# Kernel tuning notes

Hardware: AMD Instinct MI355X
Metric: run time of the kernel (lower is better)

The kernel has to match this reference:

```python
import jax, jax.numpy as jnp
import numpy as np

DIM, K, B, H, W = 256, 7, 16, 56, 56
EPS = 1e-5

def _conv(x, w, pad, groups=1):
    return jax.lax.conv_general_dilated(
        x, w, window_strides=(1, 1), padding=[(pad, pad), (pad, pad)],
        dimension_numbers=('NCHW', 'OIHW', 'NCHW'), feature_group_count=groups)

def _bn(x, g, b, m, v):
    scale = g / jnp.sqrt(v + EPS)          # [C]
    bias = b - m * scale
    return x * scale[None, :, None, None] + bias[None, :, None, None]

def _silu(x):
    return x * jax.nn.sigmoid(x)

def setup_inputs() -> dict:
    key = jax.random.key(0)
    ks = jax.random.split(key, 12)
    f = lambda k_, shp, s=0.05: jax.random.normal(k_, shp, jnp.float32) * s
    d = {
        'x':   jax.random.normal(ks[0], (B, DIM, H, W), jnp.float32),
        # RepConv branch: dense 3x3 conv + BN, dense 1x1 conv + BN
        'w3':  f(ks[1], (DIM, DIM, 3, 3)),
        'g1':  1.0 + f(ks[2], (DIM,)), 'b1': f(ks[3], (DIM,)),
        'm1':  f(ks[4], (DIM,)),       'v1': jax.random.uniform(ks[4], (DIM,), jnp.float32) + 0.5,
        'w1':  f(ks[5], (DIM, DIM, 1, 1)),
        'g2':  1.0 + f(ks[6], (DIM,)), 'b2': f(ks[7], (DIM,)),
        'm2':  f(ks[8], (DIM,)),       'v2': jax.random.uniform(ks[8], (DIM,), jnp.float32) + 0.5,
        # depthwise branches
        'dw7': f(ks[9], (DIM, 1, 7, 7)),
        'dwk': f(ks[10], (DIM, 1, K, K)),
        # final BN
        'g3':  1.0 + f(ks[11], (DIM,)), 'b3': f(ks[11], (DIM,)),
        'm3':  f(ks[11], (DIM,)),       'v3': jax.random.uniform(ks[11], (DIM,), jnp.float32) + 0.5,
    }
    return d

def reference(x, w3, g1, b1, m1, v1, w1, g2, b2, m2, v2, dw7, dwk, g3, b3, m3, v3):
    # RepConv (train-mode, bn=False): SiLU(BN(conv3x3(x)) + BN(conv1x1(x)))
    rep = _silu(_bn(_conv(x, w3, 1), g1, b1, m1, v1)
                + _bn(_conv(x, w1, 0), g2, b2, m2, v2))
    # parallel depthwise branches
    y = rep + _conv(x, dw7, 3, groups=DIM) + _conv(x, dwk, K // 2, groups=DIM)
    return _silu(_bn(y, g3, b3, m3, v3))
```

## Files before the change

### kernel.cpp

```cpp
#include <hip/hip_runtime.h>
#include <stdint.h>
#include <stddef.h>

#define DIM 256
#define NB 16
#define HH 56
#define WW 56
#define HWP (HH*WW)
#define PH 62
#define PW 62
#define NPIX (NB*HWP)
#define EPSV 1e-5f

using f32x4  = __attribute__((ext_vector_type(4))) float;
using bf16x8 = __attribute__((ext_vector_type(8))) __bf16;

static __device__ __forceinline__ unsigned short f2bf(float f) {
    union { float f; unsigned u; } v; v.f = f;
    unsigned r = v.u + 0x7FFFu + ((v.u >> 16) & 1u);
    return (unsigned short)(r >> 16);
}
static __device__ __forceinline__ float bf2f(unsigned short u) {
    union { unsigned u; float f; } v; v.u = ((unsigned)u) << 16; return v.f;
}
static __device__ __forceinline__ float silu_f(float z) {
    return z / (1.f + __expf(-z));
}

__global__ void prep_weights(
    const float* __restrict__ w3, const float* __restrict__ g1, const float* __restrict__ b1,
    const float* __restrict__ m1, const float* __restrict__ v1, const float* __restrict__ w1,
    const float* __restrict__ g2, const float* __restrict__ b2, const float* __restrict__ m2,
    const float* __restrict__ v2, const float* __restrict__ dw7, const float* __restrict__ dwk,
    const float* __restrict__ g3, const float* __restrict__ b3, const float* __restrict__ m3,
    const float* __restrict__ v3,
    unsigned short* __restrict__ WkT, float* __restrict__ dwm, float* __restrict__ biasm,
    float* __restrict__ sc3, float* __restrict__ bi3)
{
    int co = blockIdx.x, t = threadIdx.x;
    float s1 = g1[co] * rsqrtf(v1[co] + EPSV);
    float s2 = g2[co] * rsqrtf(v2[co] + EPSV);
    float w1v = w1[co*DIM + t] * s2;
    const float* w3r = w3 + (size_t)(co*DIM + t)*9;
#pragma unroll
    for (int s = 0; s < 9; ++s) {
        float v = w3r[s]*s1 + (s == 4 ? w1v : 0.f);
        WkT[((size_t)s*DIM + co)*DIM + t] = f2bf(v);
    }
    if (t < 49) dwm[co*49 + t] = dw7[co*49 + t] + dwk[co*49 + t];
    if (t == 0) {
        biasm[co] = (b1[co] - m1[co]*s1) + (b2[co] - m2[co]*s2);
        float s3 = g3[co] * rsqrtf(v3[co] + EPSV);
        sc3[co] = s3;
        bi3[co] = b3[co] - m3[co]*s3;
    }
}

__global__ void prep_xpad(const float* __restrict__ x, unsigned short* __restrict__ xpad)
{
    __shared__ float lds[64][57];
    int cc = blockIdx.x;
    int ph = blockIdx.y;
    int b  = blockIdx.z;
    int t  = threadIdx.x;
    int c0 = cc*64;
    char* rowc = (char*)xpad + ((size_t)(b*PH + ph)*PW)*(DIM*2) + c0*2;

    if (ph < 3 || ph >= HH + 3) {
        uint4 z = {0u,0u,0u,0u};
#pragma unroll
        for (int j = 0; j < 2; ++j) {
            int idx = j*256 + t;
            if (idx < 496) {
                int pix = idx >> 3, q = idx & 7;
                *(uint4*)(rowc + (size_t)pix*(DIM*2) + q*16) = z;
            }
        }
        return;
    }
    if (t < 48) {
        int p = t >> 3, q = t & 7;
        int pw = (p < 3) ? p : (PW - 6 + p);
        uint4 z = {0u,0u,0u,0u};
        *(uint4*)(rowc + (size_t)pw*(DIM*2) + q*16) = z;
    }
    int h = ph - 3;
#pragma unroll
    for (int j = 0; j < 14; ++j) {
        int idx = j*256 + t;
        int c = idx / 56, w = idx % 56;
        lds[c][w] = x[((size_t)(b*DIM + c0 + c)*HH + h)*WW + w];
    }
    __syncthreads();
#pragma unroll
    for (int j = 0; j < 7; ++j) {
        int idx = j*256 + t;
        int w = idx >> 5, cp = idx & 31;
        unsigned lo = f2bf(lds[2*cp][w]);
        unsigned hi = f2bf(lds[2*cp+1][w]);
        unsigned val = lo | (hi << 16);
        *(unsigned*)(rowc + (size_t)(w + 3)*(DIM*2) + 4*cp) = val;
    }
}

__global__ void depthwise7(const float* __restrict__ x, const float* __restrict__ dwm,
                           unsigned short* __restrict__ dwout)
{
    __shared__ float plane[PH*PW];
    int c = blockIdx.x, b = blockIdx.y, t = threadIdx.x;
    const float* xp = x + ((size_t)b*DIM + c)*HWP;
    float wr[49];
#pragma unroll
    for (int i = 0; i < 49; ++i) wr[i] = dwm[c*49 + i];
#pragma unroll
    for (int j = 0; j < 16; ++j) {
        int idx = j*256 + t;
        if (idx < PH*PW) {
            int ph = idx / PW, pw = idx % PW;
            int h = ph - 3, w = pw - 3;
            float v = 0.f;
            if ((unsigned)h < HH && (unsigned)w < WW) v = xp[h*WW + w];
            plane[idx] = v;
        }
    }
    __syncthreads();
    unsigned short* op = dwout + ((size_t)b*DIM + c)*HWP;
#pragma unroll
    for (int j = 0; j < 4; ++j) {
        int q = j*256 + t;
        if (q < 784) {
            int h = q / 14, w0 = (q % 14)*4;
            float a0=0.f, a1=0.f, a2=0.f, a3=0.f;
#pragma unroll
            for (int dy = 0; dy < 7; ++dy) {
                float row[10];
#pragma unroll
                for (int i = 0; i < 10; ++i) row[i] = plane[(h+dy)*PW + w0 + i];
#pragma unroll
                for (int dx = 0; dx < 7; ++dx) {
                    float wv = wr[dy*7 + dx];
                    a0 += row[dx]   * wv;
                    a1 += row[dx+1] * wv;
                    a2 += row[dx+2] * wv;
                    a3 += row[dx+3] * wv;
                }
            }
            uint2 pk;
            pk.x = (unsigned)f2bf(a0) | ((unsigned)f2bf(a1) << 16);
            pk.y = (unsigned)f2bf(a2) | ((unsigned)f2bf(a3) << 16);
            *(uint2*)&op[h*WW + w0] = pk;
        }
    }
}

__global__ __launch_bounds__(256, 2)
void main_conv(const unsigned short* __restrict__ xpad, const unsigned short* __restrict__ WkT,
               const unsigned short* __restrict__ dwo, const float* __restrict__ biasm,
               const float* __restrict__ sc3, const float* __restrict__ bi3,
               float* __restrict__ out)
{
    __shared__ __align__(16) char smem[65536];
    int t = threadIdx.x;
    int lane = t & 63, wv = t >> 6;
    int wm = wv >> 1, wn = wv & 1;
    int qm = lane & 15, qg = lane >> 4;

    int swz = (((lane & 7) ^ ((lane >> 3) & 7)) << 4);

    uintptr_t gA[4], gB[4];
#pragma unroll
    for (int r = 0; r < 4; ++r) {
        int pixt = r*32 + wv*8 + (lane >> 3);
        int P = blockIdx.x*128 + pixt;
        int bb = P / HWP, rem = P % HWP;
        int h = rem / WW, w = rem % WW;
        gA[r] = (uintptr_t)xpad + ((size_t)((bb*PH + h + 2)*PW + (w + 2))*DIM)*2 + swz;
        int cog = blockIdx.y*128 + pixt;
        gB[r] = (uintptr_t)WkT + ((size_t)cog*DIM)*2 + swz;
    }

    f32x4 acc[4][4] = {};

    auto stage = [&](int s, int buf) {
        int s9 = s >> 2, ch = s & 3;
        int ky = s9 / 3, kx = s9 - ky*3;
        int offA = (ky*PW + kx)*(DIM*2) + ch*128;
        int offB = s9*(DIM*DIM*2) + ch*128;
        char* base = smem + buf*32768;
#pragma unroll
        for (int r = 0; r < 4; ++r) {
            __builtin_amdgcn_global_load_lds(
                (const __attribute__((address_space(1))) void*)(gA[r] + offA),
                (__attribute__((address_space(3))) void*)(base + (r*32 + wv*8)*128),
                16, 0, 0);
            __builtin_amdgcn_global_load_lds(
                (const __attribute__((address_space(1))) void*)(gB[r] + offB),
                (__attribute__((address_space(3))) void*)(base + 16384 + (r*32 + wv*8)*128),
                16, 0, 0);
        }
    };

    int kxo = (qg << 4) ^ ((lane & 7) << 4);
    auto compute = [&](int buf) {
        const char* pA = smem + buf*32768 + (wm*64 + qm)*128;
        const char* pB = smem + buf*32768 + 16384 + (wn*64 + qm)*128;
#pragma unroll
        for (int kk = 0; kk < 2; ++kk) {
            int ko = kxo ^ (kk << 6);
            bf16x8 a[4], b[4];
#pragma unroll
            for (int i = 0; i < 4; ++i) {
                a[i] = *(const bf16x8*)(pA + i*2048 + ko);
                b[i] = *(const bf16x8*)(pB + i*2048 + ko);
            }
#pragma unroll
            for (int i = 0; i < 4; ++i)
#pragma unroll
                for (int j = 0; j < 4; ++j)
                    acc[i][j] = __builtin_amdgcn_mfma_f32_16x16x32_bf16(a[i], b[j], acc[i][j], 0, 0, 0);
        }
    };

    stage(0, 0);
    __syncthreads();
#pragma unroll 1
    for (int it = 0; it < 18; ++it) {
        stage(2*it + 1, 1);
        compute(0);
        __syncthreads();
        if (it < 17) stage(2*it + 2, 0);
        compute(1);
        __syncthreads();
    }

    float* ep = (float*)smem + wv*1088;
#pragma unroll
    for (int mi = 0; mi < 4; ++mi) {
#pragma unroll
        for (int ni = 0; ni < 4; ++ni)
#pragma unroll
            for (int r = 0; r < 4; ++r)
                ep[(ni*16 + qm)*17 + 4*qg + r] = acc[mi][ni][r];
        __syncthreads();
        int P = blockIdx.x*128 + wm*64 + mi*16 + qm;
        int bb = P / HWP, rem = P % HWP;
        size_t obase = (size_t)bb*DIM*HWP + rem;
#pragma unroll
        for (int j = 0; j < 16; ++j) {
            int col = j*4 + qg;
            int cog = blockIdx.y*128 + wn*64 + col;
            float z = ep[col*17 + qm] + biasm[cog];
            float rep = silu_f(z);
            float y = rep + bf2f(dwo[obase + (size_t)cog*HWP]);
            float yy = y * sc3[cog] + bi3[cog];
            out[obase + (size_t)cog*HWP] = silu_f(yy);
        }
        __syncthreads();
    }
}

extern "C" void kernel_launch(void* const* d_in, const int* in_sizes, int n_in,
                              void* d_out, int out_size, void* d_ws, size_t ws_size,
                              hipStream_t stream)
{
    (void)in_sizes; (void)n_in; (void)out_size; (void)ws_size;
    const float* x   = (const float*)d_in[0];
    const float* w3  = (const float*)d_in[1];
    const float* g1  = (const float*)d_in[2];
    const float* b1  = (const float*)d_in[3];
    const float* m1  = (const float*)d_in[4];
    const float* v1  = (const float*)d_in[5];
    const float* w1  = (const float*)d_in[6];
    const float* g2  = (const float*)d_in[7];
    const float* b2  = (const float*)d_in[8];
    const float* m2  = (const float*)d_in[9];
    const float* v2  = (const float*)d_in[10];
    const float* dw7 = (const float*)d_in[11];
    const float* dwk = (const float*)d_in[12];
    const float* g3  = (const float*)d_in[13];
    const float* b3  = (const float*)d_in[14];
    const float* m3  = (const float*)d_in[15];
    const float* v3  = (const float*)d_in[16];
    float* out = (float*)d_out;

    char* ws = (char*)d_ws;
    unsigned short* xpad = (unsigned short*)(ws);
    unsigned short* WkT  = (unsigned short*)(ws + 31490048);
    unsigned short* dwo  = (unsigned short*)(ws + 32669696);
    float* dwm   = (float*)(ws + 58359808);
    float* biasm = (float*)(ws + 58409984);
    float* sc3   = (float*)(ws + 58411008);
    float* bi3   = (float*)(ws + 58412032);

    prep_weights<<<dim3(DIM), dim3(256), 0, stream>>>(
        w3, g1, b1, m1, v1, w1, g2, b2, m2, v2, dw7, dwk, g3, b3, m3, v3,
        WkT, dwm, biasm, sc3, bi3);
    prep_xpad<<<dim3(4, PH, NB), dim3(256), 0, stream>>>(x, xpad);
    depthwise7<<<dim3(DIM, NB), dim3(256), 0, stream>>>(x, dwm, dwo);
    main_conv<<<dim3(NPIX/128, 2), dim3(256), 0, stream>>>(xpad, WkT, dwo, biasm, sc3, bi3, out);
}
```

Before: 166.3 us.

## Enlarge main conv block tile to 256x256 with eight waves and finer waits

```diff
diff --git a/kernel.cpp b/kernel.cpp
--- a/kernel.cpp
+++ b/kernel.cpp
@@ -153,109 +153,122 @@
     }
 }
 
-__global__ __launch_bounds__(256, 2)
+__global__ __launch_bounds__(512, 2)
 void main_conv(const unsigned short* __restrict__ xpad, const unsigned short* __restrict__ WkT,
                const unsigned short* __restrict__ dwo, const float* __restrict__ biasm,
                const float* __restrict__ sc3, const float* __restrict__ bi3,
                float* __restrict__ out)
 {
-    __shared__ __align__(16) char smem[65536];
+    __shared__ __align__(16) char smem[131072];
     int t = threadIdx.x;
     int lane = t & 63, wv = t >> 6;
-    int wm = wv >> 1, wn = wv & 1;
+    int wm = wv >> 2, wn = wv & 3;
     int qm = lane & 15, qg = lane >> 4;
-
-    int swz = (((lane & 7) ^ ((lane >> 3) & 7)) << 4);
+    int bx = blockIdx.x;
+
+    int swz = (((t & 7) ^ ((t >> 3) & 7)) << 4);
 
     uintptr_t gA[4], gB[4];
 #pragma unroll
-    for (int r = 0; r < 4; ++r) {
-        int pixt = r*32 + wv*8 + (lane >> 3);
-        int P = blockIdx.x*128 + pixt;
+    for (int p = 0; p < 4; ++p) {
+        int row = p*64 + (t >> 3);
+        int P = bx*256 + row;
         int bb = P / HWP, rem = P % HWP;
         int h = rem / WW, w = rem % WW;
-        gA[r] = (uintptr_t)xpad + ((size_t)((bb*PH + h + 2)*PW + (w + 2))*DIM)*2 + swz;
-        int cog = blockIdx.y*128 + pixt;
-        gB[r] = (uintptr_t)WkT + ((size_t)cog*DIM)*2 + swz;
-    }
-
-    f32x4 acc[4][4] = {};
+        gA[p] = (uintptr_t)xpad + ((size_t)((bb*PH + h + 2)*PW + (w + 2))*DIM)*2 + swz;
+        gB[p] = (uintptr_t)WkT + ((size_t)row*DIM)*2 + swz;
+    }
+
+    f32x4 acc[8][4] = {};
 
     auto stage = [&](int s, int buf) {
         int s9 = s >> 2, ch = s & 3;
         int ky = s9 / 3, kx = s9 - ky*3;
         int offA = (ky*PW + kx)*(DIM*2) + ch*128;
         int offB = s9*(DIM*DIM*2) + ch*128;
-        char* base = smem + buf*32768;
-#pragma unroll
-        for (int r = 0; r < 4; ++r) {
+        char* baseA = smem + buf*65536;
+        char* baseB = baseA + 32768;
+#pragma unroll
+        for (int p = 0; p < 4; ++p) {
             __builtin_amdgcn_global_load_lds(
-                (const __attribute__((address_space(1))) void*)(gA[r] + offA),
-                (__attribute__((address_space(3))) void*)(base + (r*32 + wv*8)*128),
+                (const __attribute__((address_space(1))) void*)(gA[p] + offA),
+                (__attribute__((address_space(3))) void*)(baseA + (p*64 + wv*8)*128),
                 16, 0, 0);
             __builtin_amdgcn_global_load_lds(
-                (const __attribute__((address_space(1))) void*)(gB[r] + offB),
-                (__attribute__((address_space(3))) void*)(base + 16384 + (r*32 + wv*8)*128),
+                (const __attribute__((address_space(1))) void*)(gB[p] + offB),
+                (__attribute__((address_space(3))) void*)(baseB + (p*64 + wv*8)*128),
                 16, 0, 0);
         }
     };
 
     int kxo = (qg << 4) ^ ((lane & 7) << 4);
     auto compute = [&](int buf) {
-        const char* pA = smem + buf*32768 + (wm*64 + qm)*128;
-        const char* pB = smem + buf*32768 + 16384 + (wn*64 + qm)*128;
+        const char* pA = smem + buf*65536 + (wm*128 + qm)*128;
+        const char* pB = smem + buf*65536 + 32768 + (wn*64 + qm)*128;
 #pragma unroll
         for (int kk = 0; kk < 2; ++kk) {
             int ko = kxo ^ (kk << 6);
-            bf16x8 a[4], b[4];
-#pragma unroll
-            for (int i = 0; i < 4; ++i) {
-                a[i] = *(const bf16x8*)(pA + i*2048 + ko);
-                b[i] = *(const bf16x8*)(pB + i*2048 + ko);
-            }
-#pragma unroll
-            for (int i = 0; i < 4; ++i)
+            bf16x8 a[8], b[4];
+#pragma unroll
+            for (int i = 0; i < 8; ++i) a[i] = *(const bf16x8*)(pA + i*2048 + ko);
+#pragma unroll
+            for (int j = 0; j < 4; ++j) b[j] = *(const bf16x8*)(pB + j*2048 + ko);
+#pragma unroll
+            for (int i = 0; i < 8; ++i)
 #pragma unroll
                 for (int j = 0; j < 4; ++j)
                     acc[i][j] = __builtin_amdgcn_mfma_f32_16x16x32_bf16(a[i], b[j], acc[i][j], 0, 0, 0);
         }
     };
 
+#define WAITV8() asm volatile("s_waitcnt vmcnt(8)" ::: "memory")
+#define WAITV0() asm volatile("s_waitcnt vmcnt(0)" ::: "memory")
+#define BAR()    { __builtin_amdgcn_s_barrier(); asm volatile("" ::: "memory"); }
+
     stage(0, 0);
-    __syncthreads();
 #pragma unroll 1
     for (int it = 0; it < 18; ++it) {
-        stage(2*it + 1, 1);
+        int s1 = 2*it + 1;
+        stage(s1, 1);
+        WAITV8();
+        BAR();
         compute(0);
-        __syncthreads();
-        if (it < 17) stage(2*it + 2, 0);
+        BAR();
+        if (it < 17) {
+            stage(s1 + 1, 0);
+            WAITV8();
+        } else {
+            WAITV0();
+        }
+        BAR();
         compute(1);
-        __syncthreads();
-    }
+        BAR();
+    }
+#undef WAITV8
+#undef WAITV0
+#undef BAR
 
     float* ep = (float*)smem + wv*1088;
-#pragma unroll
-    for (int mi = 0; mi < 4; ++mi) {
-#pragma unroll
-        for (int ni = 0; ni < 4; ++ni)
+#pragma unroll 1
+    for (int i = 0; i < 8; ++i) {
+#pragma unroll
+        for (int j = 0; j < 4; ++j)
 #pragma unroll
             for (int r = 0; r < 4; ++r)
-                ep[(ni*16 + qm)*17 + 4*qg + r] = acc[mi][ni][r];
-        __syncthreads();
-        int P = blockIdx.x*128 + wm*64 + mi*16 + qm;
+                ep[(j*16 + qm)*17 + 4*qg + r] = acc[i][j][r];
+        int P = bx*256 + wm*128 + i*16 + qm;
         int bb = P / HWP, rem = P % HWP;
         size_t obase = (size_t)bb*DIM*HWP + rem;
 #pragma unroll
-        for (int j = 0; j < 16; ++j) {
-            int col = j*4 + qg;
-            int cog = blockIdx.y*128 + wn*64 + col;
-            float z = ep[col*17 + qm] + biasm[cog];
+        for (int j2 = 0; j2 < 16; ++j2) {
+            int cw = j2*4 + qg;
+            int cog = wn*64 + cw;
+            float z = ep[cw*17 + qm] + biasm[cog];
             float rep = silu_f(z);
             float y = rep + bf2f(dwo[obase + (size_t)cog*HWP]);
             float yy = y * sc3[cog] + bi3[cog];
             out[obase + (size_t)cog*HWP] = silu_f(yy);
         }
-        __syncthreads();
     }
 }
 
@@ -297,5 +310,5 @@
         WkT, dwm, biasm, sc3, bi3);
     prep_xpad<<<dim3(4, PH, NB), dim3(256), 0, stream>>>(x, xpad);
     depthwise7<<<dim3(DIM, NB), dim3(256), 0, stream>>>(x, dwm, dwo);
-    main_conv<<<dim3(NPIX/128, 2), dim3(256), 0, stream>>>(xpad, WkT, dwo, biasm, sc3, bi3, out);
-}
+    main_conv<<<dim3(NPIX/256), dim3(512), 0, stream>>>(xpad, WkT, dwo, biasm, sc3, bi3, out);
+}
```

After: 180.2 us. 8.4% more time.
